# Optimization experiments

Measured on AMD Instinct MI355X. Metric: run time of the kernel, lower is better.

Reference implementation:

```python
import jax, jax.numpy as jnp
import numpy as np

N = 50000        # nodes
E = 800000       # edges
IN_C = 128       # in_channels
HID = 256        # hidden_channels
HEADS = 4
HD = HID // HEADS
LAYERS = 4
GRAPHS = 64
OUT_C = 32
MAX_POS = 10
EPS = 1e-5


def layer_norm(x, g, b):
    mu = jnp.mean(x, axis=-1, keepdims=True)
    var = jnp.mean((x - mu) ** 2, axis=-1, keepdims=True)
    return (x - mu) / jnp.sqrt(var + EPS) * g + b


def setup_inputs() -> dict:
    key = jax.random.key(0)
    ks = jax.random.split(key, 32)
    s = 0.02
    inp = {
        "x": jax.random.normal(ks[0], (N, IN_C), dtype=jnp.float32),
        "edge_index": jax.random.randint(ks[1], (2, E), 0, N, dtype=jnp.int32),
        "pos_idx": jax.random.randint(ks[2], (N,), 0, MAX_POS, dtype=jnp.int32),
        "batch": jnp.sort(jax.random.randint(ks[3], (N,), 0, GRAPHS, dtype=jnp.int32)),
        # encoder MLP: Linear(IN->HID), ReLU, LN(HID), Linear(HID->HID); weights stored [in,out]
        "enc_w1": jax.random.normal(ks[4], (IN_C, HID)) * s,
        "enc_b1": jnp.zeros((HID,), jnp.float32),
        "enc_g": jnp.ones((HID,), jnp.float32),
        "enc_beta": jnp.zeros((HID,), jnp.float32),
        "enc_w2": jax.random.normal(ks[5], (HID, HID)) * s,
        "enc_b2": jnp.zeros((HID,), jnp.float32),
        "pos_emb": jax.random.normal(ks[6], (MAX_POS, HID)) * s,
        # stacked attention-layer params [LAYERS, ...]
        "Wq": jax.random.normal(ks[7], (LAYERS, HID, HID)) * s,
        "bq": jnp.zeros((LAYERS, HID), jnp.float32),
        "Wk": jax.random.normal(ks[8], (LAYERS, HID, HID)) * s,
        "bk": jnp.zeros((LAYERS, HID), jnp.float32),
        "Wv": jax.random.normal(ks[9], (LAYERS, HID, HID)) * s,
        "bv": jnp.zeros((LAYERS, HID), jnp.float32),
        "mlp_w1": jax.random.normal(ks[10], (LAYERS, 2 * HID, HID)) * s,
        "mlp_b1": jnp.zeros((LAYERS, HID), jnp.float32),
        "mlp_g": jnp.ones((LAYERS, HID), jnp.float32),
        "mlp_beta": jnp.zeros((LAYERS, HID), jnp.float32),
        "mlp_w2": jax.random.normal(ks[11], (LAYERS, HID, HID)) * s,
        "mlp_b2": jnp.zeros((LAYERS, HID), jnp.float32),
        # classifier
        "cls_w1": jax.random.normal(ks[12], (HID, HID)) * s,
        "cls_b1": jnp.zeros((HID,), jnp.float32),
        "cls_g": jnp.ones((HID,), jnp.float32),
        "cls_beta": jnp.zeros((HID,), jnp.float32),
        "cls_w2": jax.random.normal(ks[13], (HID, OUT_C)) * s,
        "cls_b2": jnp.zeros((OUT_C,), jnp.float32),
    }
    return inp


def reference(x, edge_index, pos_idx, batch,
              enc_w1, enc_b1, enc_g, enc_beta, enc_w2, enc_b2, pos_emb,
              Wq, bq, Wk, bk, Wv, bv,
              mlp_w1, mlp_b1, mlp_g, mlp_beta, mlp_w2, mlp_b2,
              cls_w1, cls_b1, cls_g, cls_beta, cls_w2, cls_b2):
    row, col = edge_index[0], edge_index[1]
    n = x.shape[0]
    e = row.shape[0]

    # NodeEncoder
    h = layer_norm(jax.nn.relu(x @ enc_w1 + enc_b1), enc_g, enc_beta) @ enc_w2 + enc_b2
    h = h + pos_emb[pos_idx]

    scale = jnp.asarray(HD, h.dtype) ** 0.5
    for l in range(LAYERS):
        Q = (h @ Wq[l] + bq[l]).reshape(n, HEADS, HD)
        K = (h @ Wk[l] + bk[l]).reshape(n, HEADS, HD)
        V = (h @ Wv[l] + bv[l]).reshape(n, HEADS, HD)
        # per-edge attention scores [E, HEADS]
        scores = jnp.sum(Q[row] * K[col], axis=-1) / scale
        # segment softmax over destination node `row`
        m = jax.ops.segment_max(scores, row, num_segments=n)
        ex = jnp.exp(scores - m[row])
        denom = jax.ops.segment_sum(ex, row, num_segments=n)
        w = ex / denom[row]                         # [E, HEADS]
        msg = (w[..., None] * V[col]).reshape(e, HID)
        agg = jax.ops.segment_sum(msg, row, num_segments=n)  # [N, HID]
        cat = jnp.concatenate([h, agg], axis=-1)
        z = layer_norm(jax.nn.relu(cat @ mlp_w1[l] + mlp_b1[l]), mlp_g[l], mlp_beta[l]) @ mlp_w2[l] + mlp_b2[l]
        h = z + h

    # global mean pool over graphs
    sums = jax.ops.segment_sum(h, batch, num_segments=GRAPHS)
    cnt = jax.ops.segment_sum(jnp.ones((n, 1), h.dtype), batch, num_segments=GRAPHS)
    pooled = sums / jnp.maximum(cnt, 1.0)

    out = layer_norm(jax.nn.relu(pooled @ cls_w1 + cls_b1), cls_g, cls_beta) @ cls_w2 + cls_b2
    return out
```

## Files before the change

### kernel.cpp

```cpp
#include <hip/hip_runtime.h>
#include <cstdint>

#define HID 256
#define HEADS 4
#define GRAPHS 64
#define OUTC 32
#define EPSV 1e-5f
#define PSPLIT 32

typedef __bf16 b16x8 __attribute__((ext_vector_type(8)));
typedef float  f32x4 __attribute__((ext_vector_type(4)));

__device__ __forceinline__ f32x4 mfma16(b16x8 a, b16x8 b, f32x4 c) {
    return __builtin_amdgcn_mfma_f32_16x16x32_bf16(a, b, c, 0, 0, 0);
}

__device__ __forceinline__ unsigned int pack_bf16(float a, float b) {
    unsigned short ua = __builtin_bit_cast(unsigned short, (__bf16)a);
    unsigned short ub = __builtin_bit_cast(unsigned short, (__bf16)b);
    return (unsigned int)ua | ((unsigned int)ub << 16);
}

__device__ __forceinline__ void unpack2(unsigned int u, float& lo, float& hi) {
    lo = __builtin_bit_cast(float, u << 16);
    hi = __builtin_bit_cast(float, u & 0xffff0000u);
}

__device__ __forceinline__ float b2f(unsigned short u) {
    return __builtin_bit_cast(float, (unsigned int)u << 16);
}

__device__ __forceinline__ void stage_gld128(char* buf, const unsigned short* __restrict__ src,
                                             int base, int tid)
{
#pragma unroll
    for (int i = 0; i < 16; i++) {
        int idx = i * 256 + tid;
        int r = idx >> 5;
        int u = idx & 31;
        int us = u ^ (r & 7);
        const void* gp = (const void*)(src + (size_t)(base + r) * HID + us * 8);
        __builtin_amdgcn_global_load_lds(
            (const __attribute__((address_space(1))) void*)gp,
            (__attribute__((address_space(3))) void*)(buf + idx * 16),
            16, 0, 0);
    }
}

__global__ __launch_bounds__(256) void wtrans_kernel(const float* __restrict__ W,
    unsigned short* __restrict__ Wt, int K, int C)
{
    __shared__ float tile[32][33];
    const float* Wm = W + (size_t)blockIdx.z * K * C;
    unsigned short* Wtm = Wt + (size_t)blockIdx.z * K * C;
    int k0 = blockIdx.x * 32, c0 = blockIdx.y * 32;
    int tx = threadIdx.x & 31, ty = threadIdx.x >> 5;
#pragma unroll
    for (int i = 0; i < 32; i += 8)
        tile[ty + i][tx] = Wm[(size_t)(k0 + ty + i) * C + c0 + tx];
    __syncthreads();
#pragma unroll
    for (int i = 0; i < 32; i += 8) {
        float v = tile[tx][ty + i];
        Wtm[(size_t)(c0 + ty + i) * K + k0 + tx] =
            __builtin_bit_cast(unsigned short, (__bf16)v);
    }
}

__global__ __launch_bounds__(256) void enc1_mfma(
    const float* __restrict__ in0, const unsigned short* __restrict__ Wt,
    const float* __restrict__ bias, const float* __restrict__ g,
    const float* __restrict__ be, unsigned short* __restrict__ outb, int n)
{
    constexpr int KTILE = 128, ROWB = 256;
    __shared__ __align__(16) char alds[64 * 256];
    __shared__ float red[4][64][2];
    int tid = threadIdx.x, lane = tid & 63, wv = tid >> 6;
    int cg = lane & 15, rg = lane >> 4;
    int base = blockIdx.x * 64;
    int cbase = wv * 64;

    f32x4 acc[4][4];
#pragma unroll
    for (int m = 0; m < 4; m++)
#pragma unroll
        for (int f = 0; f < 4; f++) acc[m][f] = (f32x4){0.f, 0.f, 0.f, 0.f};

#pragma unroll
    for (int i = 0; i < 8; i++) {
        int idx = (i * 256 + tid) * 4;
        int row = idx >> 7, k = idx & 127;
        int node = base + row;
        float4 v = {0.f, 0.f, 0.f, 0.f};
        if (node < n) v = *(const float4*)(in0 + (size_t)node * KTILE + k);
        uint2 pp; pp.x = pack_bf16(v.x, v.y); pp.y = pack_bf16(v.z, v.w);
        int off = row * ROWB + k * 2;
        off ^= (row & 7) << 4;
        *(uint2*)(alds + off) = pp;
    }
    __syncthreads();

#pragma unroll 2
    for (int k0 = 0; k0 < KTILE; k0 += 32) {
        b16x8 a[4], b[4];
#pragma unroll
        for (int m = 0; m < 4; m++) {
            int R = m * 16 + cg;
            int off = R * ROWB + (k0 + rg * 8) * 2;
            off ^= (R & 7) << 4;
            a[m] = __builtin_bit_cast(b16x8, *(const uint4*)(alds + off));
        }
#pragma unroll
        for (int f = 0; f < 4; f++) {
            const unsigned short* p = Wt + (size_t)(cbase + f * 16 + cg) * KTILE + k0 + rg * 8;
            b[f] = __builtin_bit_cast(b16x8, *(const uint4*)p);
        }
#pragma unroll
        for (int m = 0; m < 4; m++)
#pragma unroll
            for (int f = 0; f < 4; f++)
                acc[m][f] = mfma16(a[m], b[f], acc[m][f]);
    }

    float bias_v[4], g_v[4], be_v[4];
#pragma unroll
    for (int f = 0; f < 4; f++) {
        int col = cbase + f * 16 + cg;
        bias_v[f] = bias[col]; g_v[f] = g[col]; be_v[f] = be[col];
    }
#pragma unroll
    for (int m = 0; m < 4; m++)
#pragma unroll
        for (int f = 0; f < 4; f++)
#pragma unroll
            for (int r = 0; r < 4; r++)
                acc[m][f][r] = fmaxf(acc[m][f][r] + bias_v[f], 0.f);
#pragma unroll
    for (int m = 0; m < 4; m++)
#pragma unroll
        for (int r = 0; r < 4; r++) {
            float s = acc[m][0][r] + acc[m][1][r] + acc[m][2][r] + acc[m][3][r];
            float q = acc[m][0][r] * acc[m][0][r] + acc[m][1][r] * acc[m][1][r]
                    + acc[m][2][r] * acc[m][2][r] + acc[m][3][r] * acc[m][3][r];
#pragma unroll
            for (int o = 1; o < 16; o <<= 1) {
                s += __shfl_xor(s, o, 64); q += __shfl_xor(q, o, 64);
            }
            if (cg == 0) { int R = m * 16 + rg * 4 + r; red[wv][R][0] = s; red[wv][R][1] = q; }
        }
    __syncthreads();
#pragma unroll
    for (int m = 0; m < 4; m++)
#pragma unroll
        for (int r = 0; r < 4; r++) {
            int R = m * 16 + rg * 4 + r;
            float S = red[0][R][0] + red[1][R][0] + red[2][R][0] + red[3][R][0];
            float Q = red[0][R][1] + red[1][R][1] + red[2][R][1] + red[3][R][1];
            float mu = S * (1.f / HID);
            float rs = rsqrtf(Q * (1.f / HID) - mu * mu + EPSV);
            int row = base + R;
            if (row >= n) continue;
            size_t ro = (size_t)row * HID;
#pragma unroll
            for (int f = 0; f < 4; f++) {
                float v = (acc[m][f][r] - mu) * rs * g_v[f] + be_v[f];
                outb[ro + cbase + f * 16 + cg] = __builtin_bit_cast(unsigned short, (__bf16)v);
            }
        }
}

template<int NPASS, bool RELU_LN, bool ADD_RES, bool POS>
__global__ __launch_bounds__(256) void gemm128(
    const unsigned short* __restrict__ in0, const unsigned short* __restrict__ in1,
    const unsigned short* __restrict__ Wt, const float* __restrict__ bias,
    const float* __restrict__ g, const float* __restrict__ be,
    const unsigned short* __restrict__ addsrc, const float* __restrict__ pos_emb,
    const int* __restrict__ pidx, unsigned short* __restrict__ outb, int n)
{
    constexpr int KS = 256 * NPASS;
    __shared__ __align__(16) char alds[128 * 512];
    __shared__ float red[4][128][2];

    int tid = threadIdx.x, lane = tid & 63, wv = tid >> 6;
    int cg = lane & 15, rg = lane >> 4;
    int base = blockIdx.x * 128;
    int cbase = wv * 64;

    f32x4 acc[2][4][4];
#pragma unroll
    for (int t = 0; t < 2; t++)
#pragma unroll
        for (int m = 0; m < 4; m++)
#pragma unroll
            for (int f = 0; f < 4; f++) acc[t][m][f] = (f32x4){0.f, 0.f, 0.f, 0.f};

    for (int pass = 0; pass < NPASS; pass++) {
        if (pass) __syncthreads();
        const unsigned short* src = pass ? in1 : in0;
        const unsigned short* Wp = Wt + pass * 256;

        stage_gld128(alds, src, base, tid);
        __syncthreads();

#pragma unroll
        for (int kk = 0; kk < 8; kk++) {
            b16x8 b[4];
#pragma unroll
            for (int f = 0; f < 4; f++)
                b[f] = __builtin_bit_cast(b16x8, *(const uint4*)(
                    Wp + (size_t)(cbase + f * 16 + cg) * KS + kk * 32 + rg * 8));
#pragma unroll
            for (int t = 0; t < 2; t++) {
                b16x8 a[4];
#pragma unroll
                for (int m = 0; m < 4; m++) {
                    int R = t * 64 + m * 16 + cg;
                    int off = R * 512 + (kk * 32 + rg * 8) * 2;
                    off ^= (R & 7) << 4;
                    a[m] = __builtin_bit_cast(b16x8, *(const uint4*)(alds + off));
                }
#pragma unroll
                for (int m = 0; m < 4; m++)
#pragma unroll
                    for (int f = 0; f < 4; f++)
                        acc[t][m][f] = mfma16(a[m], b[f], acc[t][m][f]);
            }
        }
    }

    float bias_v[4], g_v[4], be_v[4];
#pragma unroll
    for (int f = 0; f < 4; f++) {
        int col = cbase + f * 16 + cg;
        bias_v[f] = bias[col];
        if (RELU_LN) { g_v[f] = g[col]; be_v[f] = be[col]; }
    }
#pragma unroll
    for (int t = 0; t < 2; t++)
#pragma unroll
        for (int m = 0; m < 4; m++)
#pragma unroll
            for (int f = 0; f < 4; f++)
#pragma unroll
                for (int r = 0; r < 4; r++) acc[t][m][f][r] += bias_v[f];

    if (RELU_LN) {
#pragma unroll
        for (int t = 0; t < 2; t++)
#pragma unroll
            for (int m = 0; m < 4; m++)
#pragma unroll
                for (int f = 0; f < 4; f++)
#pragma unroll
                    for (int r = 0; r < 4; r++)
                        acc[t][m][f][r] = fmaxf(acc[t][m][f][r], 0.f);
#pragma unroll
        for (int t = 0; t < 2; t++)
#pragma unroll
            for (int m = 0; m < 4; m++)
#pragma unroll
                for (int r = 0; r < 4; r++) {
                    float s = acc[t][m][0][r] + acc[t][m][1][r] + acc[t][m][2][r] + acc[t][m][3][r];
                    float q = acc[t][m][0][r] * acc[t][m][0][r] + acc[t][m][1][r] * acc[t][m][1][r]
                            + acc[t][m][2][r] * acc[t][m][2][r] + acc[t][m][3][r] * acc[t][m][3][r];
#pragma unroll
                    for (int o = 1; o < 16; o <<= 1) {
                        s += __shfl_xor(s, o, 64); q += __shfl_xor(q, o, 64);
                    }
                    if (cg == 0) {
                        int R = t * 64 + m * 16 + rg * 4 + r;
                        red[wv][R][0] = s; red[wv][R][1] = q;
                    }
                }
        __syncthreads();
#pragma unroll
        for (int t = 0; t < 2; t++)
#pragma unroll
            for (int m = 0; m < 4; m++)
#pragma unroll
                for (int r = 0; r < 4; r++) {
                    int R = t * 64 + m * 16 + rg * 4 + r;
                    float S = red[0][R][0] + red[1][R][0] + red[2][R][0] + red[3][R][0];
                    float Q = red[0][R][1] + red[1][R][1] + red[2][R][1] + red[3][R][1];
                    float mu = S * (1.f / HID);
                    float rs = rsqrtf(Q * (1.f / HID) - mu * mu + EPSV);
#pragma unroll
                    for (int f = 0; f < 4; f++)
                        acc[t][m][f][r] = (acc[t][m][f][r] - mu) * rs * g_v[f] + be_v[f];
                }
    }

#pragma unroll
    for (int t = 0; t < 2; t++)
#pragma unroll
        for (int m = 0; m < 4; m++)
#pragma unroll
            for (int r = 0; r < 4; r++) {
                int row = base + t * 64 + m * 16 + rg * 4 + r;
                if (row >= n) continue;
                size_t ro = (size_t)row * HID;
                int pid = 0;
                if (POS) pid = pidx[row];
#pragma unroll
                for (int f = 0; f < 4; f++) {
                    int col = cbase + f * 16 + cg;
                    float v = acc[t][m][f][r];
                    if (ADD_RES) v += b2f(addsrc[ro + col]);
                    if (POS)     v += pos_emb[(size_t)pid * HID + col];
                    outb[ro + col] = __builtin_bit_cast(unsigned short, (__bf16)v);
                }
            }
}

__global__ __launch_bounds__(256) void mlp_fused(
    const unsigned short* __restrict__ h16, const unsigned short* __restrict__ a16,
    const unsigned short* __restrict__ Wt1, const float* __restrict__ b1,
    const float* __restrict__ g, const float* __restrict__ be,
    const unsigned short* __restrict__ Wt2, const float* __restrict__ b2,
    unsigned short* __restrict__ hout, int n)
{
    __shared__ __align__(16) char alds[128 * 512];
    __shared__ float red[4][128][2];
    int tid = threadIdx.x, lane = tid & 63, wv = tid >> 6;
    int cg = lane & 15, rg = lane >> 4;
    int base = blockIdx.x * 128;
    int cbase = wv * 64;

    f32x4 acc[2][4][4];
#pragma unroll
    for (int t = 0; t < 2; t++)
#pragma unroll
        for (int m = 0; m < 4; m++)
#pragma unroll
            for (int f = 0; f < 4; f++) acc[t][m][f] = (f32x4){0.f, 0.f, 0.f, 0.f};

    for (int pass = 0; pass < 2; pass++) {
        if (pass) __syncthreads();
        const unsigned short* src = pass ? a16 : h16;
        const unsigned short* Wp = Wt1 + pass * 256;
        stage_gld128(alds, src, base, tid);
        __syncthreads();
#pragma unroll
        for (int kk = 0; kk < 8; kk++) {
            b16x8 b[4];
#pragma unroll
            for (int f = 0; f < 4; f++)
                b[f] = __builtin_bit_cast(b16x8, *(const uint4*)(
                    Wp + (size_t)(cbase + f * 16 + cg) * 512 + kk * 32 + rg * 8));
#pragma unroll
            for (int t = 0; t < 2; t++) {
                b16x8 a[4];
#pragma unroll
                for (int m = 0; m < 4; m++) {
                    int R = t * 64 + m * 16 + cg;
                    int off = R * 512 + (kk * 32 + rg * 8) * 2;
                    off ^= (R & 7) << 4;
                    a[m] = __builtin_bit_cast(b16x8, *(const uint4*)(alds + off));
                }
#pragma unroll
                for (int m = 0; m < 4; m++)
#pragma unroll
                    for (int f = 0; f < 4; f++)
                        acc[t][m][f] = mfma16(a[m], b[f], acc[t][m][f]);
            }
        }
    }

    float b1_v[4], g_v[4], be_v[4];
#pragma unroll
    for (int f = 0; f < 4; f++) {
        int col = cbase + f * 16 + cg;
        b1_v[f] = b1[col]; g_v[f] = g[col]; be_v[f] = be[col];
    }
#pragma unroll
    for (int t = 0; t < 2; t++)
#pragma unroll
        for (int m = 0; m < 4; m++)
#pragma unroll
            for (int f = 0; f < 4; f++)
#pragma unroll
                for (int r = 0; r < 4; r++)
                    acc[t][m][f][r] = fmaxf(acc[t][m][f][r] + b1_v[f], 0.f);
#pragma unroll
    for (int t = 0; t < 2; t++)
#pragma unroll
        for (int m = 0; m < 4; m++)
#pragma unroll
            for (int r = 0; r < 4; r++) {
                float s = acc[t][m][0][r] + acc[t][m][1][r] + acc[t][m][2][r] + acc[t][m][3][r];
                float q = acc[t][m][0][r] * acc[t][m][0][r] + acc[t][m][1][r] * acc[t][m][1][r]
                        + acc[t][m][2][r] * acc[t][m][2][r] + acc[t][m][3][r] * acc[t][m][3][r];
#pragma unroll
                for (int o = 1; o < 16; o <<= 1) {
                    s += __shfl_xor(s, o, 64); q += __shfl_xor(q, o, 64);
                }
                if (cg == 0) {
                    int R = t * 64 + m * 16 + rg * 4 + r;
                    red[wv][R][0] = s; red[wv][R][1] = q;
                }
            }
    __syncthreads();
#pragma unroll
    for (int t = 0; t < 2; t++)
#pragma unroll
        for (int m = 0; m < 4; m++)
#pragma unroll
            for (int r = 0; r < 4; r++) {
                int R = t * 64 + m * 16 + rg * 4 + r;
                float S = red[0][R][0] + red[1][R][0] + red[2][R][0] + red[3][R][0];
                float Q = red[0][R][1] + red[1][R][1] + red[2][R][1] + red[3][R][1];
                float mu = S * (1.f / HID);
                float rs = rsqrtf(Q * (1.f / HID) - mu * mu + EPSV);
#pragma unroll
                for (int f = 0; f < 4; f++)
                    acc[t][m][f][r] = (acc[t][m][f][r] - mu) * rs * g_v[f] + be_v[f];
            }

    __syncthreads();
#pragma unroll
    for (int t = 0; t < 2; t++)
#pragma unroll
        for (int m = 0; m < 4; m++)
#pragma unroll
            for (int r = 0; r < 4; r++) {
                int R = t * 64 + m * 16 + rg * 4 + r;
#pragma unroll
                for (int f = 0; f < 4; f++) {
                    int col = cbase + f * 16 + cg;
                    int off = R * 512 + col * 2;
                    off ^= (R & 7) << 4;
                    *(unsigned short*)(alds + off) =
                        __builtin_bit_cast(unsigned short, (__bf16)acc[t][m][f][r]);
                }
            }
    __syncthreads();

#pragma unroll
    for (int t = 0; t < 2; t++)
#pragma unroll
        for (int m = 0; m < 4; m++)
#pragma unroll
            for (int f = 0; f < 4; f++) acc[t][m][f] = (f32x4){0.f, 0.f, 0.f, 0.f};
#pragma unroll
    for (int kk = 0; kk < 8; kk++) {
        b16x8 b[4];
#pragma unroll
        for (int f = 0; f < 4; f++)
            b[f] = __builtin_bit_cast(b16x8, *(const uint4*)(
                Wt2 + (size_t)(cbase + f * 16 + cg) * 256 + kk * 32 + rg * 8));
#pragma unroll
        for (int t = 0; t < 2; t++) {
            b16x8 a[4];
#pragma unroll
            for (int m = 0; m < 4; m++) {
                int R = t * 64 + m * 16 + cg;
                int off = R * 512 + (kk * 32 + rg * 8) * 2;
                off ^= (R & 7) << 4;
                a[m] = __builtin_bit_cast(b16x8, *(const uint4*)(alds + off));
            }
#pragma unroll
            for (int m = 0; m < 4; m++)
#pragma unroll
                for (int f = 0; f < 4; f++)
                    acc[t][m][f] = mfma16(a[m], b[f], acc[t][m][f]);
        }
    }

    float b2_v[4];
#pragma unroll
    for (int f = 0; f < 4; f++) b2_v[f] = b2[cbase + f * 16 + cg];
#pragma unroll
    for (int t = 0; t < 2; t++)
#pragma unroll
        for (int m = 0; m < 4; m++)
#pragma unroll
            for (int r = 0; r < 4; r++) {
                int row = base + t * 64 + m * 16 + rg * 4 + r;
                if (row >= n) continue;
                size_t ro = (size_t)row * HID;
#pragma unroll
                for (int f = 0; f < 4; f++) {
                    int col = cbase + f * 16 + cg;
                    float v = acc[t][m][f][r] + b2_v[f] + b2f(hout[ro + col]);
                    hout[ro + col] = __builtin_bit_cast(unsigned short, (__bf16)v);
                }
            }
}

__global__ __launch_bounds__(256) void qkv128_kernel(
    const unsigned short* __restrict__ hsrc,
    const unsigned short* __restrict__ Wtq, const unsigned short* __restrict__ Wtk,
    const unsigned short* __restrict__ Wtv,
    const float* __restrict__ bq, const float* __restrict__ bk, const float* __restrict__ bv,
    unsigned short* __restrict__ Qo, unsigned short* __restrict__ Ko,
    unsigned short* __restrict__ Vo, int n)
{
    __shared__ __align__(16) char alds[128 * 512];
    int tid = threadIdx.x, lane = tid & 63, wv = tid >> 6;
    int cg = lane & 15, rg = lane >> 4;
    int base = blockIdx.x * 128;
    int cbase = wv * 64;

    stage_gld128(alds, hsrc, base, tid);
    __syncthreads();

    for (int mat = 0; mat < 3; mat++) {
        const unsigned short* Wp = (mat == 0) ? Wtq : (mat == 1) ? Wtk : Wtv;
        const float* bp = (mat == 0) ? bq : (mat == 1) ? bk : bv;
        unsigned short* op = (mat == 0) ? Qo : (mat == 1) ? Ko : Vo;

        f32x4 acc[2][4][4];
#pragma unroll
        for (int t = 0; t < 2; t++)
#pragma unroll
            for (int m = 0; m < 4; m++)
#pragma unroll
                for (int f = 0; f < 4; f++) acc[t][m][f] = (f32x4){0.f, 0.f, 0.f, 0.f};

#pragma unroll
        for (int kk = 0; kk < 8; kk++) {
            b16x8 b[4];
#pragma unroll
            for (int f = 0; f < 4; f++)
                b[f] = __builtin_bit_cast(b16x8, *(const uint4*)(
                    Wp + (size_t)(cbase + f * 16 + cg) * 256 + kk * 32 + rg * 8));
#pragma unroll
            for (int t = 0; t < 2; t++) {
                b16x8 a[4];
#pragma unroll
                for (int m = 0; m < 4; m++) {
                    int R = t * 64 + m * 16 + cg;
                    int off = R * 512 + (kk * 32 + rg * 8) * 2;
                    off ^= (R & 7) << 4;
                    a[m] = __builtin_bit_cast(b16x8, *(const uint4*)(alds + off));
                }
#pragma unroll
                for (int m = 0; m < 4; m++)
#pragma unroll
                    for (int f = 0; f < 4; f++)
                        acc[t][m][f] = mfma16(a[m], b[f], acc[t][m][f]);
            }
        }

        float bias_v[4];
#pragma unroll
        for (int f = 0; f < 4; f++) bias_v[f] = bp[cbase + f * 16 + cg];
#pragma unroll
        for (int t = 0; t < 2; t++)
#pragma unroll
            for (int m = 0; m < 4; m++)
#pragma unroll
                for (int r = 0; r < 4; r++) {
                    int row = base + t * 64 + m * 16 + rg * 4 + r;
                    if (row >= n) continue;
                    size_t ro = (size_t)row * HID;
#pragma unroll
                    for (int f = 0; f < 4; f++) {
                        float v = acc[t][m][f][r] + bias_v[f];
                        op[ro + cbase + f * 16 + cg] =
                            __builtin_bit_cast(unsigned short, (__bf16)v);
                    }
                }
    }
}

__global__ void count_kernel(const int* __restrict__ row, int* __restrict__ counts, int e)
{
    int i = blockIdx.x * blockDim.x + threadIdx.x;
    if (i < e) atomicAdd(&counts[row[i]], 1);
}

__global__ __launch_bounds__(256) void scan1_kernel(const int* __restrict__ counts,
    int* __restrict__ offs, int* __restrict__ bsum, int n)
{
    __shared__ int wsumS[4];
    int tid = threadIdx.x, b = blockIdx.x;
    int i = b * 256 + tid;
    int v = (i < n) ? counts[i] : 0;
    int lane = tid & 63, wv = tid >> 6;
    int s = v;
#pragma unroll
    for (int o = 1; o < 64; o <<= 1) { int t = __shfl_up(s, o, 64); if (lane >= o) s += t; }
    if (lane == 63) wsumS[wv] = s;
    __syncthreads();
    int add = 0;
    for (int j = 0; j < wv; j++) add += wsumS[j];
    s += add;
    if (i < n) offs[i + 1] = s;
    if (tid == 255) bsum[b] = s;
}

__global__ __launch_bounds__(256) void scan2_kernel(int* __restrict__ bsum, int nb)
{
    __shared__ int wsumS[4];
    int tid = threadIdx.x;
    int v = (tid < nb) ? bsum[tid] : 0;
    int lane = tid & 63, wv = tid >> 6;
    int s = v;
#pragma unroll
    for (int o = 1; o < 64; o <<= 1) { int t = __shfl_up(s, o, 64); if (lane >= o) s += t; }
    if (lane == 63) wsumS[wv] = s;
    __syncthreads();
    int add = 0;
    for (int j = 0; j < wv; j++) add += wsumS[j];
    s += add;
    if (tid < nb) bsum[tid] = s;
}

__global__ __launch_bounds__(256) void scan3_kernel(int* __restrict__ offs,
    const int* __restrict__ bsum, int n)
{
    int tid = threadIdx.x, b = blockIdx.x;
    int i = b * 256 + tid;
    if (i == 0) offs[0] = 0;
    if (i < n && b > 0) offs[i + 1] += bsum[b - 1];
}

__global__ void scatter_kernel(const int* __restrict__ row, const int* __restrict__ col,
    const int* __restrict__ offs, int* __restrict__ cur, int* __restrict__ ccol, int e)
{
    int i = blockIdx.x * blockDim.x + threadIdx.x;
    if (i >= e) return;
    int r = row[i];
    int pos = atomicAdd(&cur[r], 1);
    ccol[offs[r] + pos] = col[i];
}

__global__ __launch_bounds__(256) void attn_hw_kernel(
    const unsigned short* __restrict__ Qm, const unsigned short* __restrict__ Km,
    const unsigned short* __restrict__ Vm,
    const int* __restrict__ offs, const int* __restrict__ ccol,
    unsigned short* __restrict__ agg, int n)
{
    int tid = threadIdx.x;
    int hw = tid >> 5;
    int l32 = tid & 31;
    int node = blockIdx.x * 8 + hw;
    if (node >= n) return;
    int start = offs[node], fin = offs[node + 1];
    size_t rowoff = (size_t)node * HID + l32 * 8;
    if (start == fin) {
        uint4 z = {0u, 0u, 0u, 0u};
        *(uint4*)(agg + rowoff) = z;
        return;
    }

    uint4 qr = *(const uint4*)(Qm + rowoff);
    float qf[8];
    unpack2(qr.x, qf[0], qf[1]);
    unpack2(qr.y, qf[2], qf[3]);
    unpack2(qr.z, qf[4], qf[5]);
    unpack2(qr.w, qf[6], qf[7]);

    float m = -3.0e38f, d = 0.f;
    float acc[8];
#pragma unroll
    for (int j = 0; j < 8; j++) acc[j] = 0.f;

    int c0 = ccol[start];
    int c1 = (start + 1 < fin) ? ccol[start + 1] : c0;
    uint4 krA = *(const uint4*)(Km + (size_t)c0 * HID + l32 * 8);
    uint4 vrA = *(const uint4*)(Vm + (size_t)c0 * HID + l32 * 8);
    uint4 krB = *(const uint4*)(Km + (size_t)c1 * HID + l32 * 8);
    uint4 vrB = *(const uint4*)(Vm + (size_t)c1 * HID + l32 * 8);

    for (int i = start; i < fin; i++) {
        uint4 kr = krA, vr = vrA;
        krA = krB; vrA = vrB;
        int ip = i + 2;
        if (ip < fin) {
            int c = ccol[ip];
            krB = *(const uint4*)(Km + (size_t)c * HID + l32 * 8);
            vrB = *(const uint4*)(Vm + (size_t)c * HID + l32 * 8);
        }
        float k0, k1, k2, k3, k4, k5, k6, k7;
        unpack2(kr.x, k0, k1); unpack2(kr.y, k2, k3);
        unpack2(kr.z, k4, k5); unpack2(kr.w, k6, k7);
        float p = qf[0] * k0 + qf[1] * k1 + qf[2] * k2 + qf[3] * k3
                + qf[4] * k4 + qf[5] * k5 + qf[6] * k6 + qf[7] * k7;
        p += __shfl_xor(p, 1, 64);
        p += __shfl_xor(p, 2, 64);
        p += __shfl_xor(p, 4, 64);
        float s = p * 0.125f;
        float mn = fmaxf(m, s);
        float sc = __expf(m - mn);
        float w = __expf(s - mn);
        d = d * sc + w;
        float v0, v1, v2, v3, v4, v5, v6, v7;
        unpack2(vr.x, v0, v1); unpack2(vr.y, v2, v3);
        unpack2(vr.z, v4, v5); unpack2(vr.w, v6, v7);
        acc[0] = acc[0] * sc + w * v0;  acc[1] = acc[1] * sc + w * v1;
        acc[2] = acc[2] * sc + w * v2;  acc[3] = acc[3] * sc + w * v3;
        acc[4] = acc[4] * sc + w * v4;  acc[5] = acc[5] * sc + w * v5;
        acc[6] = acc[6] * sc + w * v6;  acc[7] = acc[7] * sc + w * v7;
        m = mn;
    }

    float inv = 1.f / d;
    uint4 out;
    out.x = pack_bf16(acc[0] * inv, acc[1] * inv);
    out.y = pack_bf16(acc[2] * inv, acc[3] * inv);
    out.z = pack_bf16(acc[4] * inv, acc[5] * inv);
    out.w = pack_bf16(acc[6] * inv, acc[7] * inv);
    *(uint4*)(agg + rowoff) = out;
}

__global__ void bounds_kernel(const int* __restrict__ batch, int* __restrict__ gb, int n)
{
    int g = threadIdx.x;
    if (g > GRAPHS) return;
    int lo = 0, hi = n;
    while (lo < hi) { int mid = (lo + hi) >> 1; if (batch[mid] < g) lo = mid + 1; else hi = mid; }
    gb[g] = lo;
}

__global__ __launch_bounds__(256) void pool_partial_kernel(
    const unsigned short* __restrict__ h16,
    const int* __restrict__ gb, float* __restrict__ partial)
{
    int s = blockIdx.x, g = blockIdx.y, tid = threadIdx.x;
    int lo = gb[g], hi = gb[g + 1];
    float sum = 0.f;
    for (int i = lo + s; i < hi; i += PSPLIT)
        sum += b2f(h16[(size_t)i * HID + tid]);
    partial[((size_t)g * PSPLIT + s) * HID + tid] = sum;
}

__global__ __launch_bounds__(256) void pool_reduce_kernel(const float* __restrict__ partial,
    const int* __restrict__ gb, float* __restrict__ pooled)
{
    int g = blockIdx.x, tid = threadIdx.x;
    float sum = 0.f;
#pragma unroll
    for (int s = 0; s < PSPLIT; s++) sum += partial[((size_t)g * PSPLIT + s) * HID + tid];
    int cnt = gb[g + 1] - gb[g];
    pooled[g * HID + tid] = sum / fmaxf((float)cnt, 1.f);
}

__global__ __launch_bounds__(256) void cls_kernel(const float* __restrict__ pooled,
    const float* __restrict__ W1, const float* __restrict__ b1,
    const float* __restrict__ g, const float* __restrict__ be,
    const float* __restrict__ W2, const float* __restrict__ b2,
    float* __restrict__ out)
{
    __shared__ float pin[HID];
    __shared__ float hbuf[HID];
    __shared__ float red2[4][2];
    int tid = threadIdx.x, gi = blockIdx.x;
    int lane = tid & 63, wv = tid >> 6;
    pin[tid] = pooled[gi * HID + tid];
    __syncthreads();
    float acc = 0.f;
    for (int k = 0; k < HID; k++) acc += pin[k] * W1[k * HID + tid];
    acc = fmaxf(acc + b1[tid], 0.f);
    float s = acc, q = acc * acc;
#pragma unroll
    for (int o = 1; o < 64; o <<= 1) { s += __shfl_xor(s, o, 64); q += __shfl_xor(q, o, 64); }
    if (lane == 0) { red2[wv][0] = s; red2[wv][1] = q; }
    __syncthreads();
    float S = red2[0][0] + red2[1][0] + red2[2][0] + red2[3][0];
    float Q = red2[0][1] + red2[1][1] + red2[2][1] + red2[3][1];
    float mu = S * (1.f / HID);
    float rs = rsqrtf(Q * (1.f / HID) - mu * mu + EPSV);
    hbuf[tid] = (acc - mu) * rs * g[tid] + be[tid];
    __syncthreads();
    if (tid < OUTC) {
        float o = 0.f;
        for (int k = 0; k < HID; k++) o += hbuf[k] * W2[k * OUTC + tid];
        out[gi * OUTC + tid] = o + b2[tid];
    }
}

extern "C" void kernel_launch(void* const* d_in, const int* in_sizes, int n_in,
                              void* d_out, int out_size, void* d_ws, size_t ws_size,
                              hipStream_t stream)
{
    const float* x        = (const float*)d_in[0];
    const int*   ei       = (const int*)d_in[1];
    const int*   pidx     = (const int*)d_in[2];
    const int*   batch    = (const int*)d_in[3];
    const float* enc_w1   = (const float*)d_in[4];
    const float* enc_b1   = (const float*)d_in[5];
    const float* enc_g    = (const float*)d_in[6];
    const float* enc_beta = (const float*)d_in[7];
    const float* enc_w2   = (const float*)d_in[8];
    const float* enc_b2   = (const float*)d_in[9];
    const float* pos_emb  = (const float*)d_in[10];
    const float* Wq       = (const float*)d_in[11];
    const float* bq       = (const float*)d_in[12];
    const float* Wk       = (const float*)d_in[13];
    const float* bk       = (const float*)d_in[14];
    const float* Wv       = (const float*)d_in[15];
    const float* bv       = (const float*)d_in[16];
    const float* mlp_w1   = (const float*)d_in[17];
    const float* mlp_b1   = (const float*)d_in[18];
    const float* mlp_g    = (const float*)d_in[19];
    const float* mlp_beta = (const float*)d_in[20];
    const float* mlp_w2   = (const float*)d_in[21];
    const float* mlp_b2   = (const float*)d_in[22];
    const float* cls_w1   = (const float*)d_in[23];
    const float* cls_b1   = (const float*)d_in[24];
    const float* cls_g    = (const float*)d_in[25];
    const float* cls_beta = (const float*)d_in[26];
    const float* cls_w2   = (const float*)d_in[27];
    const float* cls_b2   = (const float*)d_in[28];

    int n = in_sizes[2];
    int e = in_sizes[1] / 2;
    const int* row = ei;
    const int* col = ei + e;

    char* p = (char*)d_ws;
    auto alloc = [&](size_t bytes) -> void* {
        void* r = (void*)p;
        p += (bytes + 255) & ~(size_t)255;
        return r;
    };
    size_t NH = (size_t)n * HID;
    unsigned short* h16  = (unsigned short*)alloc(NH * 2);
    unsigned short* a16  = (unsigned short*)alloc(NH * 2);
    unsigned short* m16  = (unsigned short*)alloc(NH * 2);
    unsigned short* Qb   = (unsigned short*)alloc(NH * 2);
    unsigned short* Kb   = (unsigned short*)alloc(NH * 2);
    unsigned short* Vb   = (unsigned short*)alloc(NH * 2);
    float* partial = (float*)alloc((size_t)GRAPHS * PSPLIT * HID * 4);
    float* pooled  = (float*)alloc((size_t)GRAPHS * HID * 4);
    int* counts = (int*)alloc((size_t)n * 4);
    int* offs   = (int*)alloc((size_t)(n + 1) * 4);
    int* cur    = (int*)alloc((size_t)n * 4);
    int* ccol   = (int*)alloc((size_t)e * 4);
    int* bsum   = (int*)alloc(1024);
    int* gb     = (int*)alloc((GRAPHS + 1) * 4);
    unsigned short* wt_e1 = (unsigned short*)alloc((size_t)128 * 256 * 2);
    unsigned short* wt_e2 = (unsigned short*)alloc((size_t)256 * 256 * 2);
    unsigned short* wt_q  = (unsigned short*)alloc((size_t)4 * 256 * 256 * 2);
    unsigned short* wt_k  = (unsigned short*)alloc((size_t)4 * 256 * 256 * 2);
    unsigned short* wt_v  = (unsigned short*)alloc((size_t)4 * 256 * 256 * 2);
    unsigned short* wt_m1 = (unsigned short*)alloc((size_t)4 * 512 * 256 * 2);
    unsigned short* wt_m2 = (unsigned short*)alloc((size_t)4 * 256 * 256 * 2);

    int gblocks64  = (n + 63) / 64;
    int gblocks128 = (n + 127) / 128;
    int nb = (n + 255) / 256;

    wtrans_kernel<<<dim3(4, 8, 1),  256, 0, stream>>>(enc_w1, wt_e1, 128, 256);
    wtrans_kernel<<<dim3(8, 8, 1),  256, 0, stream>>>(enc_w2, wt_e2, 256, 256);
    wtrans_kernel<<<dim3(8, 8, 4),  256, 0, stream>>>(Wq,     wt_q,  256, 256);
    wtrans_kernel<<<dim3(8, 8, 4),  256, 0, stream>>>(Wk,     wt_k,  256, 256);
    wtrans_kernel<<<dim3(8, 8, 4),  256, 0, stream>>>(Wv,     wt_v,  256, 256);
    wtrans_kernel<<<dim3(16, 8, 4), 256, 0, stream>>>(mlp_w1, wt_m1, 512, 256);
    wtrans_kernel<<<dim3(8, 8, 4),  256, 0, stream>>>(mlp_w2, wt_m2, 256, 256);

    hipMemsetAsync(counts, 0, (size_t)n * 4, stream);
    hipMemsetAsync(cur, 0, (size_t)n * 4, stream);
    count_kernel<<<(e + 255) / 256, 256, 0, stream>>>(row, counts, e);
    scan1_kernel<<<nb, 256, 0, stream>>>(counts, offs, bsum, n);
    scan2_kernel<<<1, 256, 0, stream>>>(bsum, nb);
    scan3_kernel<<<nb, 256, 0, stream>>>(offs, bsum, n);
    scatter_kernel<<<(e + 255) / 256, 256, 0, stream>>>(row, col, offs, cur, ccol, e);
    bounds_kernel<<<1, 128, 0, stream>>>(batch, gb, n);

    enc1_mfma<<<gblocks64, 256, 0, stream>>>(x, wt_e1, enc_b1, enc_g, enc_beta, m16, n);
    gemm128<1, false, false, true><<<gblocks128, 256, 0, stream>>>(
        m16, nullptr, wt_e2, enc_b2, nullptr, nullptr, nullptr, pos_emb, pidx, h16, n);

    int ablocks = (n + 7) / 8;
    for (int l = 0; l < 4; l++) {
        size_t wo = (size_t)l * 256 * 256;
        size_t bo = (size_t)l * HID;
        qkv128_kernel<<<gblocks128, 256, 0, stream>>>(
            h16, wt_q + wo, wt_k + wo, wt_v + wo, bq + bo, bk + bo, bv + bo,
            Qb, Kb, Vb, n);
        attn_hw_kernel<<<ablocks, 256, 0, stream>>>(Qb, Kb, Vb, offs, ccol, a16, n);
        mlp_fused<<<gblocks128, 256, 0, stream>>>(
            h16, a16, wt_m1 + (size_t)l * 512 * 256, mlp_b1 + bo,
            mlp_g + bo, mlp_beta + bo, wt_m2 + wo, mlp_b2 + bo, h16, n);
    }

    pool_partial_kernel<<<dim3(PSPLIT, GRAPHS), 256, 0, stream>>>(h16, gb, partial);
    pool_reduce_kernel<<<GRAPHS, 256, 0, stream>>>(partial, gb, pooled);
    cls_kernel<<<GRAPHS, 256, 0, stream>>>(pooled, cls_w1, cls_b1, cls_g, cls_beta,
                                           cls_w2, cls_b2, (float*)d_out);
}
```

Before: 1.249 ms.

## Merge weight transposes, split QKV projection across grid, drop attention prefetch

All seven weight transpose launches are merged into one kernel that picks its matrix from blockIdx.z, which removes launch overhead. The QKV projection now puts Q, K and V on a second grid dimension, giving three times as many blocks with less work each, at the cost of staging the h tile three times. The attention kernel's two-deep software prefetch of K/V rows is removed in favour of plain per-edge loads, which lowers register pressure but exposes gather latency.

```diff
diff --git a/kernel.cpp b/kernel.cpp
--- a/kernel.cpp
+++ b/kernel.cpp
@@ -47,23 +47,42 @@
     }
 }
 
-__global__ __launch_bounds__(256) void wtrans_kernel(const float* __restrict__ W,
-    unsigned short* __restrict__ Wt, int K, int C)
+__global__ __launch_bounds__(256) void wtrans_all(
+    const float* __restrict__ e1, const float* __restrict__ e2,
+    const float* __restrict__ q,  const float* __restrict__ k,
+    const float* __restrict__ v,  const float* __restrict__ m1,
+    const float* __restrict__ m2,
+    unsigned short* __restrict__ we1, unsigned short* __restrict__ we2,
+    unsigned short* __restrict__ wq,  unsigned short* __restrict__ wk,
+    unsigned short* __restrict__ wv,  unsigned short* __restrict__ wm1,
+    unsigned short* __restrict__ wm2)
 {
     __shared__ float tile[32][33];
-    const float* Wm = W + (size_t)blockIdx.z * K * C;
-    unsigned short* Wtm = Wt + (size_t)blockIdx.z * K * C;
-    int k0 = blockIdx.x * 32, c0 = blockIdx.y * 32;
+    int z = blockIdx.z;
+    const float* W; unsigned short* Wt; int K; int mat = 0;
+    if (z == 0)      { W = e1; Wt = we1; K = 128; }
+    else if (z == 1) { W = e2; Wt = we2; K = 256; }
+    else if (z < 6)  { W = q;  Wt = wq;  K = 256; mat = z - 2; }
+    else if (z < 10) { W = k;  Wt = wk;  K = 256; mat = z - 6; }
+    else if (z < 14) { W = v;  Wt = wv;  K = 256; mat = z - 10; }
+    else if (z < 18) { W = m1; Wt = wm1; K = 512; mat = z - 14; }
+    else             { W = m2; Wt = wm2; K = 256; mat = z - 18; }
+    int k0 = blockIdx.x * 32;
+    if (k0 >= K) return;
+    const int C = 256;
+    W  += (size_t)mat * K * C;
+    Wt += (size_t)mat * K * C;
+    int c0 = blockIdx.y * 32;
     int tx = threadIdx.x & 31, ty = threadIdx.x >> 5;
 #pragma unroll
     for (int i = 0; i < 32; i += 8)
-        tile[ty + i][tx] = Wm[(size_t)(k0 + ty + i) * C + c0 + tx];
+        tile[ty + i][tx] = W[(size_t)(k0 + ty + i) * C + c0 + tx];
     __syncthreads();
 #pragma unroll
     for (int i = 0; i < 32; i += 8) {
-        float v = tile[tx][ty + i];
-        Wtm[(size_t)(c0 + ty + i) * K + k0 + tx] =
-            __builtin_bit_cast(unsigned short, (__bf16)v);
+        float vv = tile[tx][ty + i];
+        Wt[(size_t)(c0 + ty + i) * K + k0 + tx] =
+            __builtin_bit_cast(unsigned short, (__bf16)vv);
     }
 }
 
@@ -500,68 +519,66 @@
     int cg = lane & 15, rg = lane >> 4;
     int base = blockIdx.x * 128;
     int cbase = wv * 64;
+    int mat = blockIdx.y;
+    const unsigned short* Wp = (mat == 0) ? Wtq : (mat == 1) ? Wtk : Wtv;
+    const float* bp = (mat == 0) ? bq : (mat == 1) ? bk : bv;
+    unsigned short* op = (mat == 0) ? Qo : (mat == 1) ? Ko : Vo;
 
     stage_gld128(alds, hsrc, base, tid);
     __syncthreads();
 
-    for (int mat = 0; mat < 3; mat++) {
-        const unsigned short* Wp = (mat == 0) ? Wtq : (mat == 1) ? Wtk : Wtv;
-        const float* bp = (mat == 0) ? bq : (mat == 1) ? bk : bv;
-        unsigned short* op = (mat == 0) ? Qo : (mat == 1) ? Ko : Vo;
-
-        f32x4 acc[2][4][4];
-#pragma unroll
-        for (int t = 0; t < 2; t++)
+    f32x4 acc[2][4][4];
+#pragma unroll
+    for (int t = 0; t < 2; t++)
+#pragma unroll
+        for (int m = 0; m < 4; m++)
+#pragma unroll
+            for (int f = 0; f < 4; f++) acc[t][m][f] = (f32x4){0.f, 0.f, 0.f, 0.f};
+
+#pragma unroll
+    for (int kk = 0; kk < 8; kk++) {
+        b16x8 b[4];
+#pragma unroll
+        for (int f = 0; f < 4; f++)
+            b[f] = __builtin_bit_cast(b16x8, *(const uint4*)(
+                Wp + (size_t)(cbase + f * 16 + cg) * 256 + kk * 32 + rg * 8));
+#pragma unroll
+        for (int t = 0; t < 2; t++) {
+            b16x8 a[4];
+#pragma unroll
+            for (int m = 0; m < 4; m++) {
+                int R = t * 64 + m * 16 + cg;
+                int off = R * 512 + (kk * 32 + rg * 8) * 2;
+                off ^= (R & 7) << 4;
+                a[m] = __builtin_bit_cast(b16x8, *(const uint4*)(alds + off));
+            }
 #pragma unroll
             for (int m = 0; m < 4; m++)
 #pragma unroll
-                for (int f = 0; f < 4; f++) acc[t][m][f] = (f32x4){0.f, 0.f, 0.f, 0.f};
-
-#pragma unroll
-        for (int kk = 0; kk < 8; kk++) {
-            b16x8 b[4];
-#pragma unroll
-            for (int f = 0; f < 4; f++)
-                b[f] = __builtin_bit_cast(b16x8, *(const uint4*)(
-                    Wp + (size_t)(cbase + f * 16 + cg) * 256 + kk * 32 + rg * 8));
-#pragma unroll
-            for (int t = 0; t < 2; t++) {
-                b16x8 a[4];
-#pragma unroll
-                for (int m = 0; m < 4; m++) {
-                    int R = t * 64 + m * 16 + cg;
-                    int off = R * 512 + (kk * 32 + rg * 8) * 2;
-                    off ^= (R & 7) << 4;
-                    a[m] = __builtin_bit_cast(b16x8, *(const uint4*)(alds + off));
-                }
-#pragma unroll
-                for (int m = 0; m < 4; m++)
-#pragma unroll
-                    for (int f = 0; f < 4; f++)
-                        acc[t][m][f] = mfma16(a[m], b[f], acc[t][m][f]);
-            }
+                for (int f = 0; f < 4; f++)
+                    acc[t][m][f] = mfma16(a[m], b[f], acc[t][m][f]);
         }
-
-        float bias_v[4];
-#pragma unroll
-        for (int f = 0; f < 4; f++) bias_v[f] = bp[cbase + f * 16 + cg];
-#pragma unroll
-        for (int t = 0; t < 2; t++)
-#pragma unroll
-            for (int m = 0; m < 4; m++)
-#pragma unroll
-                for (int r = 0; r < 4; r++) {
-                    int row = base + t * 64 + m * 16 + rg * 4 + r;
-                    if (row >= n) continue;
-                    size_t ro = (size_t)row * HID;
-#pragma unroll
-                    for (int f = 0; f < 4; f++) {
-                        float v = acc[t][m][f][r] + bias_v[f];
-                        op[ro + cbase + f * 16 + cg] =
-                            __builtin_bit_cast(unsigned short, (__bf16)v);
-                    }
-                }
-    }
+    }
+
+    float bias_v[4];
+#pragma unroll
+    for (int f = 0; f < 4; f++) bias_v[f] = bp[cbase + f * 16 + cg];
+#pragma unroll
+    for (int t = 0; t < 2; t++)
+#pragma unroll
+        for (int m = 0; m < 4; m++)
+#pragma unroll
+            for (int r = 0; r < 4; r++) {
+                int row = base + t * 64 + m * 16 + rg * 4 + r;
+                if (row >= n) continue;
+                size_t ro = (size_t)row * HID;
+#pragma unroll
+                for (int f = 0; f < 4; f++) {
+                    float v = acc[t][m][f][r] + bias_v[f];
+                    op[ro + cbase + f * 16 + cg] =
+                        __builtin_bit_cast(unsigned short, (__bf16)v);
+                }
+            }
 }
 
 __global__ void count_kernel(const int* __restrict__ row, int* __restrict__ counts, int e)
@@ -657,22 +674,12 @@
 #pragma unroll
     for (int j = 0; j < 8; j++) acc[j] = 0.f;
 
-    int c0 = ccol[start];
-    int c1 = (start + 1 < fin) ? ccol[start + 1] : c0;
-    uint4 krA = *(const uint4*)(Km + (size_t)c0 * HID + l32 * 8);
-    uint4 vrA = *(const uint4*)(Vm + (size_t)c0 * HID + l32 * 8);
-    uint4 krB = *(const uint4*)(Km + (size_t)c1 * HID + l32 * 8);
-    uint4 vrB = *(const uint4*)(Vm + (size_t)c1 * HID + l32 * 8);
-
     for (int i = start; i < fin; i++) {
-        uint4 kr = krA, vr = vrA;
-        krA = krB; vrA = vrB;
-        int ip = i + 2;
-        if (ip < fin) {
-            int c = ccol[ip];
-            krB = *(const uint4*)(Km + (size_t)c * HID + l32 * 8);
-            vrB = *(const uint4*)(Vm + (size_t)c * HID + l32 * 8);
-        }
+        int c = ccol[i];
+        const unsigned short* kp = Km + (size_t)c * HID + l32 * 8;
+        const unsigned short* vp = Vm + (size_t)c * HID + l32 * 8;
+        uint4 kr = *(const uint4*)kp;
+        uint4 vr = *(const uint4*)vp;
         float k0, k1, k2, k3, k4, k5, k6, k7;
         unpack2(kr.x, k0, k1); unpack2(kr.y, k2, k3);
         unpack2(kr.z, k4, k5); unpack2(kr.w, k6, k7);
@@ -843,13 +850,9 @@
     int gblocks128 = (n + 127) / 128;
     int nb = (n + 255) / 256;
 
-    wtrans_kernel<<<dim3(4, 8, 1),  256, 0, stream>>>(enc_w1, wt_e1, 128, 256);
-    wtrans_kernel<<<dim3(8, 8, 1),  256, 0, stream>>>(enc_w2, wt_e2, 256, 256);
-    wtrans_kernel<<<dim3(8, 8, 4),  256, 0, stream>>>(Wq,     wt_q,  256, 256);
-    wtrans_kernel<<<dim3(8, 8, 4),  256, 0, stream>>>(Wk,     wt_k,  256, 256);
-    wtrans_kernel<<<dim3(8, 8, 4),  256, 0, stream>>>(Wv,     wt_v,  256, 256);
-    wtrans_kernel<<<dim3(16, 8, 4), 256, 0, stream>>>(mlp_w1, wt_m1, 512, 256);
-    wtrans_kernel<<<dim3(8, 8, 4),  256, 0, stream>>>(mlp_w2, wt_m2, 256, 256);
+    wtrans_all<<<dim3(16, 8, 22), 256, 0, stream>>>(
+        enc_w1, enc_w2, Wq, Wk, Wv, mlp_w1, mlp_w2,
+        wt_e1, wt_e2, wt_q, wt_k, wt_v, wt_m1, wt_m2);
 
     hipMemsetAsync(counts, 0, (size_t)n * 4, stream);
     hipMemsetAsync(cur, 0, (size_t)n * 4, stream);
@@ -868,7 +871,7 @@
     for (int l = 0; l < 4; l++) {
         size_t wo = (size_t)l * 256 * 256;
         size_t bo = (size_t)l * HID;
-        qkv128_kernel<<<gblocks128, 256, 0, stream>>>(
+        qkv128_kernel<<<dim3(gblocks128, 3), 256, 0, stream>>>(
             h16, wt_q + wo, wt_k + wo, wt_v + wo, bq + bo, bk + bo, bv + bo,
             Qb, Kb, Vb, n);
         attn_hw_kernel<<<ablocks, 256, 0, stream>>>(Qb, Kb, Vb, offs, ccol, a16, n);
```

Result: faster. 1.184 ms (-5.2%).
